# Kernel tuning notes

Hardware: AMD Instinct MI355X
Metric: run time of the kernel (lower is better)

Reference implementation:

```python
import jax, jax.numpy as jnp
import numpy as np

B, S, H, W, C = 1, 14, 56, 56, 192
WS = 7            # cubic window
SH = 3            # shift
HEADS = 6
HD = C // HEADS
N = WS ** 3       # 343 tokens per window
NW = (S // WS) * (H // WS) * (W // WS)  # 128 windows
SCALE = HD ** -0.5
HID = 4 * C
TBL = (2 * WS - 1) ** 3  # 2197


def _rel_index():
    # faithful to torch: meshgrid with indexing='xy' and the (3*ws-1)/(2*ws-1) strides
    c = np.stack(np.meshgrid(np.arange(WS), np.arange(WS), np.arange(WS), indexing='xy'))
    f = c.reshape(3, -1)                      # (3, N)
    r = (f[:, :, None] - f[:, None, :]).transpose(1, 2, 0)  # (N, N, 3)
    r = r + (WS - 1)
    r[..., 0] *= 3 * WS - 1
    r[..., 1] *= 2 * WS - 1
    return jnp.asarray(r.sum(-1), dtype=jnp.int32)  # (N, N)

REL_IDX = _rel_index()


def _ln(x, g, b):
    m = x.mean(-1, keepdims=True)
    v = ((x - m) ** 2).mean(-1, keepdims=True)
    return (x - m) * jax.lax.rsqrt(v + 1e-5) * g + b


def _partition(x):  # (B,S,H,W,C) -> (B*nW, N, C)
    x = x.reshape(B, S // WS, WS, H // WS, WS, W // WS, WS, C)
    x = x.transpose(0, 1, 3, 5, 2, 4, 6, 7)
    return x.reshape(-1, N, C)


def _reverse(w):  # (B*nW, N, C) -> (B,S,H,W,C)
    x = w.reshape(B, S // WS, H // WS, W // WS, WS, WS, WS, C)
    x = x.transpose(0, 1, 4, 2, 5, 3, 6, 7)
    return x.reshape(B, S, H, W, C)


def setup_inputs() -> dict:
    key = jax.random.key(0)
    ks = jax.random.split(key, 16)
    L = S * H * W
    p = lambda k, shp, s=0.02: (jax.random.normal(k, shp, dtype=jnp.float32) * s)
    return {
        'x': jax.random.normal(ks[0], (B, L, C), dtype=jnp.float32),
        'mask_matrix': jax.random.normal(ks[1], (NW, N, N), dtype=jnp.float32),
        'skip': jax.random.normal(ks[2], (B, L, C), dtype=jnp.float32),
        'x_up': jax.random.normal(ks[3], (B, L, C), dtype=jnp.float32),
        'norm1_g': jnp.ones((C,), jnp.float32),
        'norm1_b': jnp.zeros((C,), jnp.float32),
        'kv_w': p(ks[4], (C, 2 * C)),
        'kv_b': jnp.zeros((2 * C,), jnp.float32),
        'rel_bias_table': p(ks[5], (TBL, HEADS)),
        'proj_w': p(ks[6], (C, C)),
        'proj_b': jnp.zeros((C,), jnp.float32),
        'norm2_g': jnp.ones((C,), jnp.float32),
        'norm2_b': jnp.zeros((C,), jnp.float32),
        'fc1_w': p(ks[7], (C, HID)),
        'fc1_b': jnp.zeros((HID,), jnp.float32),
        'fc2_w': p(ks[8], (HID, C)),
        'fc2_b': jnp.zeros((C,), jnp.float32),
    }


def reference(x, mask_matrix, skip, x_up, norm1_g, norm1_b, kv_w, kv_b,
              rel_bias_table, proj_w, proj_b, norm2_g, norm2_b,
              fc1_w, fc1_b, fc2_w, fc2_b):
    shortcut = x
    sk = _ln(skip, norm1_g, norm1_b).reshape(B, S, H, W, C)
    xu = _ln(x_up, norm1_g, norm1_b).reshape(B, S, H, W, C)
    # cyclic shift (shift_size > 0, dims divisible by window -> no padding)
    sk = jnp.roll(sk, (-SH, -SH, -SH), axis=(1, 2, 3))
    xu = jnp.roll(xu, (-SH, -SH, -SH), axis=(1, 2, 3))
    sk_w = _partition(sk)   # (Bw, N, C)
    xu_w = _partition(xu)
    Bw = sk_w.shape[0]
    kv = (sk_w @ kv_w + kv_b).reshape(Bw, N, 2, HEADS, HD)
    k = kv[:, :, 0].transpose(0, 2, 1, 3)   # (Bw, h, N, d)
    v = kv[:, :, 1].transpose(0, 2, 1, 3)
    q = xu_w.reshape(Bw, N, HEADS, HD).transpose(0, 2, 1, 3) * SCALE
    attn = jnp.einsum('bhnd,bhmd->bhnm', q, k)
    bias = rel_bias_table[REL_IDX].transpose(2, 0, 1)  # (h, N, N)
    attn = attn + bias[None]
    attn = attn.reshape(B, NW, HEADS, N, N) + mask_matrix[None, :, None]
    attn = jax.nn.softmax(attn.reshape(Bw, HEADS, N, N), axis=-1)
    out = jnp.einsum('bhnm,bhmd->bhnd', attn, v)
    out = out.transpose(0, 2, 1, 3).reshape(Bw, N, C)
    out = out @ proj_w + proj_b
    xr = _reverse(out)
    xr = jnp.roll(xr, (SH, SH, SH), axis=(1, 2, 3)).reshape(B, S * H * W, C)
    x = shortcut + xr
    h = _ln(x, norm2_g, norm2_b)
    h = jax.nn.gelu(h @ fc1_w + fc1_b, approximate=False) @ fc2_w + fc2_b
    return x + h
```

## Files before the change

### kernel.cpp

```cpp
#include <hip/hip_runtime.h>
#include <cstddef>

typedef unsigned short u16;
typedef unsigned int   u32;
typedef __bf16 bf16_t;
typedef bf16_t bf16x8 __attribute__((ext_vector_type(8)));
typedef short  s16x4  __attribute__((ext_vector_type(4)));
typedef float  f32x4  __attribute__((ext_vector_type(4)));
typedef u16    u16x4  __attribute__((ext_vector_type(4)));

#define NPAD 352
#define VTS  352
#define LOG2E 1.4426950408889634f
#define RESCALE_THR 11.5f

__device__ __forceinline__ u16 f2b(float f) {
  return __builtin_bit_cast(u16, (__bf16)f);
}
__device__ __forceinline__ float b2f(u16 h) {
  return __uint_as_float(((u32)h) << 16);
}
__device__ __forceinline__ float fexp2(float x) {
#if __has_builtin(__builtin_amdgcn_exp2f)
  return __builtin_amdgcn_exp2f(x);
#else
  float r; asm("v_exp_f32 %0, %1" : "=v"(r) : "v"(x)); return r;
#endif
}
__device__ __forceinline__ f32x4 mfma16(bf16x8 a, bf16x8 b, f32x4 c) {
  return __builtin_amdgcn_mfma_f32_16x16x32_bf16(a, b, c, 0, 0, 0);
}
__device__ __forceinline__ f32x4 mfma16x16(s16x4 a, s16x4 b, f32x4 c) {
#if __has_builtin(__builtin_amdgcn_mfma_f32_16x16x16bf16_1k)
  return __builtin_amdgcn_mfma_f32_16x16x16bf16_1k(a, b, c, 0, 0, 0);
#else
  f32x4 d;
  asm volatile("v_mfma_f32_16x16x16_bf16 %0, %1, %2, %3"
               : "=&v"(d) : "v"(a), "v"(b), "v"(c));
  return d;
#endif
}
__device__ __forceinline__ void gl_lds16(const void* g, void* l) {
  __builtin_amdgcn_global_load_lds((const __attribute__((address_space(1))) void*)g,
                                   (__attribute__((address_space(3))) void*)l, 16, 0, 0);
}

__device__ __forceinline__ int win_to_global(int w, int n) {
  int ws = w >> 6, wh = (w >> 3) & 7, ww = w & 7;
  int ts = (n * 1338) >> 16;
  int rem = n - ts * 49;
  int th = (rem * 9363) >> 16;
  int tw = rem - th * 7;
  int gs = ws * 7 + ts + 3; if (gs >= 14) gs -= 14;
  int gh = wh * 7 + th + 3; if (gh >= 56) gh -= 56;
  int gw = ww * 7 + tw + 3; if (gw >= 56) gw -= 56;
  return (gs * 56 + gh) * 56 + gw;
}

#define MC_END 15488
#define LN_END (MC_END + 10976)
#define WC_END (LN_END + 1824)
#define PRE_GRID (WC_END + 726)

__global__ __launch_bounds__(256) void k_pre(
    const float* __restrict__ mask, u16* __restrict__ mb,
    const float* __restrict__ skip, const float* __restrict__ xup,
    const float* __restrict__ g1, const float* __restrict__ b1,
    u16* __restrict__ skw, u16* __restrict__ qb,
    const float* __restrict__ kv_w, const float* __restrict__ proj_w,
    const float* __restrict__ fc1_w, const float* __restrict__ fc2_w,
    u16* kvT, u16* projT, u16* fc1T, u16* fc2T,
    const float* __restrict__ tbl, u16* __restrict__ bf) {
  int bid = blockIdx.x, tid = threadIdx.x;
  if (bid < MC_END) {
    int t = bid * 256 + tid;
    int w = t / (352 * 88);
    int r = t - w * (352 * 88);
    int n = r / 88;
    int q = r - n * 88;
    u16x4 v = {0, 0, 0, 0};
    if (n < 343) {
      const float* src = mask + ((size_t)w * 343 + n) * 343 + q * 4;
      #pragma unroll
      for (int j = 0; j < 4; ++j) if (q * 4 + j < 343) v[j] = f2b(src[j] * LOG2E);
    }
    *(u16x4*)&mb[((size_t)w * 352 + n) * 352 + q * 4] = v;
  } else if (bid < LN_END) {
    int wid = tid >> 6, lane = tid & 63;
    int m = (bid - MC_END) * 4 + wid;
    u32 w = ((u32)m * 48914u) >> 24;
    int n = m - (int)w * 343;
    int g = win_to_global((int)w, n);
    float xs[3], xu[3];
    float s1 = 0.f, s2 = 0.f, t1 = 0.f, t2 = 0.f;
    #pragma unroll
    for (int i = 0; i < 3; ++i) {
      int c = lane + i * 64;
      xs[i] = skip[(size_t)g * 192 + c];
      xu[i] = xup[(size_t)g * 192 + c];
      s1 += xs[i]; s2 += xs[i] * xs[i];
      t1 += xu[i]; t2 += xu[i] * xu[i];
    }
    #pragma unroll
    for (int off = 1; off < 64; off <<= 1) {
      s1 += __shfl_xor(s1, off); s2 += __shfl_xor(s2, off);
      t1 += __shfl_xor(t1, off); t2 += __shfl_xor(t2, off);
    }
    const float inv = 1.f / 192.f;
    float ms = s1 * inv, vs = s2 * inv - ms * ms;
    float mu = t1 * inv, vu = t2 * inv - mu * mu;
    float rs = rsqrtf(vs + 1e-5f), ru = rsqrtf(vu + 1e-5f);
    #pragma unroll
    for (int i = 0; i < 3; ++i) {
      int c = lane + i * 64;
      float gg = g1[c], bb = b1[c];
      skw[(size_t)m * 192 + c] = f2b((xs[i] - ms) * rs * gg + bb);
      float qv = ((xu[i] - mu) * ru * gg + bb) * 0.25503513f;
      int h = c >> 5, d = c & 31;
      qb[(size_t)(((int)w * 6 + h) * NPAD + n) * 32 + d] = f2b(qv);
    }
  } else if (bid < WC_END) {
    int t = (bid - LN_END) * 256 + tid;
    if (t < 384 * 192) { int nn = t / 192, kk = t - nn * 192; kvT[t] = f2b(kv_w[kk * 384 + nn]); return; }
    t -= 384 * 192;
    if (t < 256 * 192) { int nn = t / 192, kk = t - nn * 192; projT[t] = (nn < 192) ? f2b(proj_w[kk * 192 + nn]) : (u16)0; return; }
    t -= 256 * 192;
    if (t < 768 * 192) { int nn = t / 192, kk = t - nn * 192; fc1T[t] = f2b(fc1_w[kk * 768 + nn]); return; }
    t -= 768 * 192;
    if (t < 256 * 768) { int nn = t / 768, kk = t - nn * 768; fc2T[t] = (nn < 192) ? f2b(fc2_w[kk * 192 + nn]) : (u16)0; return; }
  } else {
    int t = (bid - WC_END) * 256 + tid;
    int h = t / (352 * 88);
    int r = t - h * (352 * 88);
    int n = r / 88;
    int q = r - n * 88;
    u16x4 v = {0, 0, 0, 0};
    if (n < 343 && h < 6) {
      int tsn = (n * 1338) >> 16, remn = n - tsn * 49, thn = (remn * 9363) >> 16, twn = remn - thn * 7;
      #pragma unroll
      for (int j = 0; j < 4; ++j) {
        int m = q * 4 + j;
        if (m < 343) {
          int tsm = (m * 1338) >> 16, remm = m - tsm * 49, thm = (remm * 9363) >> 16, twm = remm - thm * 7;
          int idx = (thn - thm) * 20 + (tsn - tsm) * 13 + (twn - twm) + 204;
          v[j] = f2b(tbl[idx * 6 + h] * LOG2E);
        }
      }
    }
    if (h < 6) *(u16x4*)&bf[((size_t)h * 352 + n) * 352 + q * 4] = v;
  }
}

__global__ __launch_bounds__(256) void k_ln2(const float* __restrict__ xr,
    const float* __restrict__ g2, const float* __restrict__ b2, u16* __restrict__ o) {
  int wid = threadIdx.x >> 6, lane = threadIdx.x & 63;
  int m = blockIdx.x * 4 + wid;
  float v[3]; float s1 = 0.f, s2 = 0.f;
  #pragma unroll
  for (int i = 0; i < 3; ++i) {
    int c = lane + i * 64;
    v[i] = xr[(size_t)m * 192 + c];
    s1 += v[i]; s2 += v[i] * v[i];
  }
  #pragma unroll
  for (int off = 1; off < 64; off <<= 1) { s1 += __shfl_xor(s1, off); s2 += __shfl_xor(s2, off); }
  const float inv = 1.f / 192.f;
  float ms = s1 * inv, vs = s2 * inv - ms * ms;
  float rs = rsqrtf(vs + 1e-5f);
  #pragma unroll
  for (int i = 0; i < 3; ++i) {
    int c = lane + i * 64;
    o[(size_t)m * 192 + c] = f2b((v[i] - ms) * rs * g2[c] + b2[c]);
  }
}

template<int EPI>
__global__ __launch_bounds__(256) void k_gemm(
    const u16* __restrict__ A, const u16* __restrict__ Bm, int K, int nbn,
    const float* __restrict__ bias,
    u16* __restrict__ outa, u16* __restrict__ outb,
    const float* __restrict__ xin, float* __restrict__ xres,
    float* __restrict__ outf) {
  __shared__ __align__(16) u16 As[128 * 32];
  __shared__ __align__(16) u16 Bs[128 * 32];
  int bid = blockIdx.x;
  int xcd = bid & 7, j = bid >> 3;
  int bn = j % nbn, bmL = j / nbn;
  int bm = xcd * 43 + bmL;
  if (bm >= 343) return;
  int tid = threadIdx.x;
  int wid = tid >> 6, lane = tid & 63, lr = lane & 15, lg = lane >> 4;
  int wr = wid >> 1, wc = wid & 1;
  f32x4 acc[4][4] = {};
  const u16* Abase = A + (size_t)bm * 128 * K;
  const u16* Bbase = Bm + (size_t)bn * 128 * K;
  int nk = K >> 5;
  for (int kt = 0; kt < nk; ++kt) {
    int ci0 = tid, ci1 = tid + 256;
    int r0 = ci0 >> 2, c0 = (ci0 & 3) * 8;
    int r1 = ci1 >> 2, c1 = (ci1 & 3) * 8;
    gl_lds16(Abase + (size_t)r0 * K + kt * 32 + c0, &As[ci0 * 8]);
    gl_lds16(Abase + (size_t)r1 * K + kt * 32 + c1, &As[ci1 * 8]);
    gl_lds16(Bbase + (size_t)r0 * K + kt * 32 + c0, &Bs[ci0 * 8]);
    gl_lds16(Bbase + (size_t)r1 * K + kt * 32 + c1, &Bs[ci1 * 8]);
    __syncthreads();
    bf16x8 af[4], bfr[4];
    #pragma unroll
    for (int mi = 0; mi < 4; ++mi) af[mi] = *(const bf16x8*)&As[(wr * 64 + mi * 16 + lr) * 32 + lg * 8];
    #pragma unroll
    for (int ni = 0; ni < 4; ++ni) bfr[ni] = *(const bf16x8*)&Bs[(wc * 64 + ni * 16 + lr) * 32 + lg * 8];
    #pragma unroll
    for (int mi = 0; mi < 4; ++mi)
      #pragma unroll
      for (int ni = 0; ni < 4; ++ni)
        acc[mi][ni] = mfma16(af[mi], bfr[ni], acc[mi][ni]);
    __syncthreads();
  }
  #pragma unroll
  for (int mi = 0; mi < 4; ++mi) {
    #pragma unroll
    for (int r = 0; r < 4; ++r) {
      int grow = bm * 128 + wr * 64 + mi * 16 + lg * 4 + r;
      if (EPI == 0) {
        u32 w = ((u32)grow * 48914u) >> 24; int n = grow - (int)w * 343;
        #pragma unroll
        for (int ni = 0; ni < 4; ++ni) {
          int gcol = bn * 128 + wc * 64 + ni * 16 + lr;
          float v = acc[mi][ni][r] + bias[gcol];
          if (gcol < 192) {
            int hh = gcol >> 5, d = gcol & 31;
            int dswz = ((((d >> 3) ^ ((n >> 1) & 3)) << 3) | (d & 7));
            outa[(size_t)(((int)w * 6 + hh) * NPAD + n) * 32 + dswz] = f2b(v);
          } else {
            int c2 = gcol - 192; int hh = c2 >> 5, d = c2 & 31;
            int nswz = ((((n >> 3) ^ ((d >> 1) & 3)) << 3) | (n & 7));
            outb[(size_t)(((int)w * 6 + hh) * 32 + d) * VTS + nswz] = f2b(v);
          }
        }
      } else if (EPI == 1) {
        #pragma unroll
        for (int ni = 0; ni < 4; ++ni) {
          int gcol = bn * 128 + wc * 64 + ni * 16 + lr;
          if (gcol < 192) {
            float v = acc[mi][ni][r] + bias[gcol] + xin[(size_t)grow * 192 + gcol];
            xres[(size_t)grow * 192 + gcol] = v;
          }
        }
      } else if (EPI == 2) {
        #pragma unroll
        for (int ni = 0; ni < 4; ++ni) {
          int gcol = bn * 128 + wc * 64 + ni * 16 + lr;
          float v = acc[mi][ni][r] + bias[gcol];
          v = 0.5f * v * (1.f + erff(v * 0.7071067811865476f));
          outa[(size_t)grow * 768 + gcol] = f2b(v);
        }
      } else {
        #pragma unroll
        for (int ni = 0; ni < 4; ++ni) {
          int gcol = bn * 128 + wc * 64 + ni * 16 + lr;
          if (gcol < 192)
            outf[(size_t)grow * 192 + gcol] = acc[mi][ni][r] + bias[gcol] + xin[(size_t)grow * 192 + gcol];
        }
      }
    }
  }
}

template<int CT0, int LEN, bool TAIL, bool FIRST>
__device__ __forceinline__ void attn_chunk(const u16* __restrict__ Ks, const u16* __restrict__ Vs,
    bf16x8 qa, int lr, int lg, int swz,
    const u16* __restrict__ brow, const u16* __restrict__ mrow,
    f32x4& o0, f32x4& o1, float& mrun, float& sum) {
  u16x4 bb[LEN], mm[LEN];
  #pragma unroll
  for (int j = 0; j < LEN; ++j) {
    bb[j] = *(const u16x4*)&brow[(CT0 + j) * 16];
    mm[j] = *(const u16x4*)&mrow[(CT0 + j) * 16];
  }
  f32x4 s[LEN];
  const f32x4 z = {0.f, 0.f, 0.f, 0.f};
  __builtin_amdgcn_s_setprio(1);
  #pragma unroll
  for (int j = 0; j < LEN; ++j) {
    bf16x8 kf = *(const bf16x8*)&Ks[((CT0 + j) * 16 + lr) * 32 + (lg ^ swz) * 8];
    s[j] = mfma16(kf, qa, z);
  }
  __builtin_amdgcn_s_setprio(0);
  #pragma unroll
  for (int j = 0; j < LEN; ++j)
    #pragma unroll
    for (int r = 0; r < 4; ++r) s[j][r] += b2f(bb[j][r]) + b2f(mm[j][r]);
  if (TAIL) {
    int m0 = 336 + lg * 4;
    #pragma unroll
    for (int r = 0; r < 4; ++r) if (m0 + r >= 343) s[LEN - 1][r] = -1e30f;
  }
  float mloc = -1e30f;
  #pragma unroll
  for (int j = 0; j < LEN; ++j)
    mloc = fmaxf(mloc, fmaxf(fmaxf(s[j][0], s[j][1]), fmaxf(s[j][2], s[j][3])));
  if (FIRST) {
    mloc = fmaxf(mloc, __shfl_xor(mloc, 16));
    mloc = fmaxf(mloc, __shfl_xor(mloc, 32));
    mrun = mloc;
  } else if (!__all(mloc <= mrun + RESCALE_THR)) {
    mloc = fmaxf(mloc, __shfl_xor(mloc, 16));
    mloc = fmaxf(mloc, __shfl_xor(mloc, 32));
    float mnew = fmaxf(mrun, mloc);
    float sc = fexp2(mrun - mnew);
    #pragma unroll
    for (int r = 0; r < 4; ++r) {
      float scr = __shfl(sc, lg * 4 + r);
      o0[r] *= scr; o1[r] *= scr;
    }
    sum *= sc;
    mrun = mnew;
  }
  #pragma unroll
  for (int j = 0; j < LEN; ++j)
    #pragma unroll
    for (int r = 0; r < 4; ++r) { float p = fexp2(s[j][r] - mrun); s[j][r] = p; sum += p; }
  __builtin_amdgcn_s_setprio(1);
  #pragma unroll
  for (int j = 0; j < LEN; ++j) {
    s16x4 pa;
    #pragma unroll
    for (int r = 0; r < 4; ++r) pa[r] = (short)f2b(s[j][r]);
    int c16 = 2 * (CT0 + j) + (lg >> 1);
    int vo = ((c16 ^ swz) * 8) + (lg & 1) * 4;
    s16x4 v0 = *(const s16x4*)&Vs[lr * 352 + vo];
    s16x4 v1 = *(const s16x4*)&Vs[(16 + lr) * 352 + vo];
    o0 = mfma16x16(pa, v0, o0);
    o1 = mfma16x16(pa, v1, o1);
  }
  __builtin_amdgcn_s_setprio(0);
}

__global__ __launch_bounds__(256) void k_attn(const u16* __restrict__ qb, const u16* __restrict__ kb,
    const u16* __restrict__ vtb, const u16* __restrict__ bfull, const u16* __restrict__ maskbf,
    u16* __restrict__ att) {
  __shared__ __align__(16) u16 Ks[352 * 32];
  __shared__ __align__(16) u16 Vs[32 * 352];
  __shared__ __align__(16) u16 Ot[4][16][40];
  int bid = blockIdx.x;
  int xcd = bid & 7, i = bid >> 3;
  int wl = i / 6, h = i - wl * 6;
  int w = xcd * 16 + wl;
  int tid = threadIdx.x, wid = tid >> 6, lane = tid & 63, lr = lane & 15, lg = lane >> 4;
  const u16* Q  = qb  + (size_t)(w * 6 + h) * NPAD * 32;
  const u16* Kg = kb  + (size_t)(w * 6 + h) * NPAD * 32;
  const u16* Vg = vtb + (size_t)(w * 6 + h) * 32 * VTS;
  const u16* Bp = bfull + (size_t)h * 352 * 352;
  const u16* Mp = maskbf + (size_t)w * 352 * 352;
  #pragma unroll
  for (int it = 0; it < 11; ++it) {
    int idx = it * 256 + tid;
    if (idx < 1408) gl_lds16(Kg + idx * 8, &Ks[idx * 8]);
    else            gl_lds16(Vg + (idx - 1408) * 8, &Vs[(idx - 1408) * 8]);
  }
  __syncthreads();
  int swz = (lr >> 1) & 3;
  for (int rt = wid; rt < 22; rt += 4) {
    int n = rt * 16 + lr;
    bf16x8 qa = *(const bf16x8*)&Q[(size_t)n * 32 + lg * 8];
    const u16* brow = Bp + (size_t)n * 352 + lg * 4;
    const u16* mrow = Mp + (size_t)n * 352 + lg * 4;
    f32x4 o0 = {0.f, 0.f, 0.f, 0.f}, o1 = {0.f, 0.f, 0.f, 0.f};
    float mrun = -1e30f, sum = 0.f;
    attn_chunk<0,  6, false, true >(Ks, Vs, qa, lr, lg, swz, brow, mrow, o0, o1, mrun, sum);
    attn_chunk<6,  6, false, false>(Ks, Vs, qa, lr, lg, swz, brow, mrow, o0, o1, mrun, sum);
    attn_chunk<12, 6, false, false>(Ks, Vs, qa, lr, lg, swz, brow, mrow, o0, o1, mrun, sum);
    attn_chunk<18, 4, true,  false>(Ks, Vs, qa, lr, lg, swz, brow, mrow, o0, o1, mrun, sum);
    sum += __shfl_xor(sum, 16);
    sum += __shfl_xor(sum, 32);
    float rs = 1.f / sum;
    #pragma unroll
    for (int r = 0; r < 4; ++r) {
      float rsr = __shfl(rs, lg * 4 + r);
      Ot[wid][lg * 4 + r][lr] = f2b(o0[r] * rsr);
      Ot[wid][lg * 4 + r][16 + lr] = f2b(o1[r] * rsr);
    }
    if (n < 343) {
      int g = win_to_global(w, n);
      bf16x8 ov = *(const bf16x8*)&Ot[wid][lr][lg * 8];
      *(bf16x8*)&att[(size_t)g * 192 + h * 32 + lg * 8] = ov;
    }
  }
}

static const size_t OFF_W    = 0;
static const size_t OFF_XRES = (size_t)1 << 20;
static const size_t OFF_MASK = OFF_XRES;
static const size_t OFF_LN2  = OFF_XRES + ((size_t)34 << 20);
static const size_t OFF_SKW  = OFF_LN2  + ((size_t)17 << 20);
static const size_t OFF_Q    = OFF_SKW  + ((size_t)17 << 20);
static const size_t OFF_K    = OFF_Q    + ((size_t)17 << 20);
static const size_t OFF_VT   = OFF_K    + ((size_t)17 << 20);
static const size_t OFF_ATT  = OFF_VT   + ((size_t)17 << 20);
static const size_t OFF_BIAS = OFF_ATT  + ((size_t)17 << 20);
static const size_t OFF_FC1  = OFF_SKW;

extern "C" void kernel_launch(void* const* d_in, const int* in_sizes, int n_in,
                              void* d_out, int out_size, void* d_ws, size_t ws_size,
                              hipStream_t stream) {
  const float* x      = (const float*)d_in[0];
  const float* mask   = (const float*)d_in[1];
  const float* skip   = (const float*)d_in[2];
  const float* xup    = (const float*)d_in[3];
  const float* n1g    = (const float*)d_in[4];
  const float* n1b    = (const float*)d_in[5];
  const float* kv_w   = (const float*)d_in[6];
  const float* kv_b   = (const float*)d_in[7];
  const float* tbl    = (const float*)d_in[8];
  const float* proj_w = (const float*)d_in[9];
  const float* proj_b = (const float*)d_in[10];
  const float* n2g    = (const float*)d_in[11];
  const float* n2b    = (const float*)d_in[12];
  const float* fc1_w  = (const float*)d_in[13];
  const float* fc1_b  = (const float*)d_in[14];
  const float* fc2_w  = (const float*)d_in[15];
  const float* fc2_b  = (const float*)d_in[16];
  char* ws = (char*)d_ws;
  u16* kvT   = (u16*)(ws + OFF_W);
  u16* projT = kvT + 384 * 192;
  u16* fc1T  = projT + 256 * 192;
  u16* fc2T  = fc1T + 768 * 192;
  float* xres = (float*)(ws + OFF_XRES);
  u16* maskbf = (u16*)(ws + OFF_MASK);
  u16* ln2o  = (u16*)(ws + OFF_LN2);
  u16* skw   = (u16*)(ws + OFF_SKW);
  u16* qb    = (u16*)(ws + OFF_Q);
  u16* kb    = (u16*)(ws + OFF_K);
  u16* vt    = (u16*)(ws + OFF_VT);
  u16* att   = (u16*)(ws + OFF_ATT);
  u16* bfull = (u16*)(ws + OFF_BIAS);
  u16* fc1o  = (u16*)(ws + OFF_FC1);
  float* outp = (float*)d_out;

  k_pre<<<dim3(PRE_GRID), dim3(256), 0, stream>>>(
      mask, maskbf, skip, xup, n1g, n1b, skw, qb,
      kv_w, proj_w, fc1_w, fc2_w, kvT, projT, fc1T, fc2T, tbl, bfull);
  k_gemm<0><<<dim3(8 * 43 * 3), dim3(256), 0, stream>>>(skw, kvT, 192, 3, kv_b, kb, vt, nullptr, nullptr, nullptr);
  k_attn<<<dim3(768), dim3(256), 0, stream>>>(qb, kb, vt, bfull, maskbf, att);
  k_gemm<1><<<dim3(8 * 43 * 2), dim3(256), 0, stream>>>(att, projT, 192, 2, proj_b, nullptr, nullptr, x, xres, nullptr);
  k_ln2<<<dim3(10976), dim3(256), 0, stream>>>(xres, n2g, n2b, ln2o);
  k_gemm<2><<<dim3(8 * 43 * 6), dim3(256), 0, stream>>>(ln2o, fc1T, 192, 6, fc1_b, fc1o, nullptr, nullptr, nullptr, nullptr);
  k_gemm<3><<<dim3(8 * 43 * 2), dim3(256), 0, stream>>>(fc1o, fc2T, 768, 2, fc2_b, nullptr, nullptr, xres, nullptr, outp);
}
```

Baseline: 305.2 us.

## Fuse fc1+GELU+fc2 MLP into one kernel keeping hidden activations in LDS

```diff
diff --git a/kernel.cpp b/kernel.cpp
--- a/kernel.cpp
+++ b/kernel.cpp
@@ -246,21 +246,94 @@
             xres[(size_t)grow * 192 + gcol] = v;
           }
         }
-      } else if (EPI == 2) {
+      }
+    }
+  }
+}
+
+__global__ __launch_bounds__(256) void k_mlp(
+    const u16* __restrict__ A, const u16* __restrict__ W1, const u16* __restrict__ W2,
+    const float* __restrict__ fb1, const float* __restrict__ fb2,
+    const float* __restrict__ xres, float* __restrict__ outp) {
+  __shared__ __align__(16) u16 As[128 * 32];
+  __shared__ __align__(16) u16 Bs[128 * 32];
+  __shared__ __align__(16) u16 Hs[128 * 136];
+  int bid = blockIdx.x;
+  int xcd = bid & 7, bmL = bid >> 3;
+  int bm = xcd * 43 + bmL;
+  if (bm >= 343) return;
+  int tid = threadIdx.x;
+  int wid = tid >> 6, lane = tid & 63, lr = lane & 15, lg = lane >> 4;
+  int wr = wid >> 1, wc = wid & 1;
+  f32x4 acc2[4][6] = {};
+  const u16* Abase = A + (size_t)bm * 128 * 192;
+  for (int hc = 0; hc < 6; ++hc) {
+    f32x4 acc1[4][4] = {};
+    const u16* W1c = W1 + (size_t)hc * 128 * 192;
+    for (int kt = 0; kt < 6; ++kt) {
+      int ci0 = tid, ci1 = tid + 256;
+      int r0 = ci0 >> 2, c0 = (ci0 & 3) * 8;
+      int r1 = ci1 >> 2, c1 = (ci1 & 3) * 8;
+      gl_lds16(Abase + (size_t)r0 * 192 + kt * 32 + c0, &As[ci0 * 8]);
+      gl_lds16(Abase + (size_t)r1 * 192 + kt * 32 + c1, &As[ci1 * 8]);
+      gl_lds16(W1c + (size_t)r0 * 192 + kt * 32 + c0, &Bs[ci0 * 8]);
+      gl_lds16(W1c + (size_t)r1 * 192 + kt * 32 + c1, &Bs[ci1 * 8]);
+      __syncthreads();
+      bf16x8 af[4], bfr[4];
+      #pragma unroll
+      for (int mi = 0; mi < 4; ++mi) af[mi] = *(const bf16x8*)&As[(wr * 64 + mi * 16 + lr) * 32 + lg * 8];
+      #pragma unroll
+      for (int ni = 0; ni < 4; ++ni) bfr[ni] = *(const bf16x8*)&Bs[(wc * 64 + ni * 16 + lr) * 32 + lg * 8];
+      #pragma unroll
+      for (int mi = 0; mi < 4; ++mi)
+        #pragma unroll
+        for (int ni = 0; ni < 4; ++ni)
+          acc1[mi][ni] = mfma16(af[mi], bfr[ni], acc1[mi][ni]);
+      __syncthreads();
+    }
+    #pragma unroll
+    for (int mi = 0; mi < 4; ++mi) {
+      #pragma unroll
+      for (int r = 0; r < 4; ++r) {
+        int rowL = wr * 64 + mi * 16 + lg * 4 + r;
         #pragma unroll
         for (int ni = 0; ni < 4; ++ni) {
-          int gcol = bn * 128 + wc * 64 + ni * 16 + lr;
-          float v = acc[mi][ni][r] + bias[gcol];
+          int hcol = wc * 64 + ni * 16 + lr;
+          float v = acc1[mi][ni][r] + fb1[hc * 128 + hcol];
           v = 0.5f * v * (1.f + erff(v * 0.7071067811865476f));
-          outa[(size_t)grow * 768 + gcol] = f2b(v);
+          Hs[rowL * 136 + hcol] = f2b(v);
         }
-      } else {
+      }
+    }
+    __syncthreads();
+    __builtin_amdgcn_s_setprio(1);
+    #pragma unroll
+    for (int kt2 = 0; kt2 < 4; ++kt2) {
+      bf16x8 hf[4], wf[6];
+      #pragma unroll
+      for (int mi = 0; mi < 4; ++mi)
+        hf[mi] = *(const bf16x8*)&Hs[(wr * 64 + mi * 16 + lr) * 136 + kt2 * 32 + lg * 8];
+      #pragma unroll
+      for (int ni = 0; ni < 6; ++ni)
+        wf[ni] = *(const bf16x8*)&W2[(size_t)(wc * 96 + ni * 16 + lr) * 768 + hc * 128 + kt2 * 32 + lg * 8];
+      #pragma unroll
+      for (int mi = 0; mi < 4; ++mi)
         #pragma unroll
-        for (int ni = 0; ni < 4; ++ni) {
-          int gcol = bn * 128 + wc * 64 + ni * 16 + lr;
-          if (gcol < 192)
-            outf[(size_t)grow * 192 + gcol] = acc[mi][ni][r] + bias[gcol] + xin[(size_t)grow * 192 + gcol];
-        }
+        for (int ni = 0; ni < 6; ++ni)
+          acc2[mi][ni] = mfma16(hf[mi], wf[ni], acc2[mi][ni]);
+    }
+    __builtin_amdgcn_s_setprio(0);
+    __syncthreads();
+  }
+  #pragma unroll
+  for (int mi = 0; mi < 4; ++mi) {
+    #pragma unroll
+    for (int r = 0; r < 4; ++r) {
+      int grow = bm * 128 + wr * 64 + mi * 16 + lg * 4 + r;
+      #pragma unroll
+      for (int ni = 0; ni < 6; ++ni) {
+        int gcol = wc * 96 + ni * 16 + lr;
+        outp[(size_t)grow * 192 + gcol] = acc2[mi][ni][r] + fb2[gcol] + xres[(size_t)grow * 192 + gcol];
       }
     }
   }
@@ -398,7 +471,6 @@
 static const size_t OFF_VT   = OFF_K    + ((size_t)17 << 20);
 static const size_t OFF_ATT  = OFF_VT   + ((size_t)17 << 20);
 static const size_t OFF_BIAS = OFF_ATT  + ((size_t)17 << 20);
-static const size_t OFF_FC1  = OFF_SKW;
 
 extern "C" void kernel_launch(void* const* d_in, const int* in_sizes, int n_in,
                               void* d_out, int out_size, void* d_ws, size_t ws_size,
@@ -434,7 +506,6 @@
   u16* vt    = (u16*)(ws + OFF_VT);
   u16* att   = (u16*)(ws + OFF_ATT);
   u16* bfull = (u16*)(ws + OFF_BIAS);
-  u16* fc1o  = (u16*)(ws + OFF_FC1);
   float* outp = (float*)d_out;
 
   k_pre<<<dim3(PRE_GRID), dim3(256), 0, stream>>>(
@@ -444,6 +515,5 @@
   k_attn<<<dim3(768), dim3(256), 0, stream>>>(qb, kb, vt, bfull, maskbf, att);
   k_gemm<1><<<dim3(8 * 43 * 2), dim3(256), 0, stream>>>(att, projT, 192, 2, proj_b, nullptr, nullptr, x, xres, nullptr);
   k_ln2<<<dim3(10976), dim3(256), 0, stream>>>(xres, n2g, n2b, ln2o);
-  k_gemm<2><<<dim3(8 * 43 * 6), dim3(256), 0, stream>>>(ln2o, fc1T, 192, 6, fc1_b, fc1o, nullptr, nullptr, nullptr, nullptr);
-  k_gemm<3><<<dim3(8 * 43 * 2), dim3(256), 0, stream>>>(fc1o, fc2T, 768, 2, fc2_b, nullptr, nullptr, xres, nullptr, outp);
-}
+  k_mlp<<<dim3(344), dim3(256), 0, stream>>>(ln2o, fc1T, fc2T, fc1_b, fc2_b, xres, outp);
+}
```

Result: slower. 360.1 us (+18.0%).
